# Kernel tuning notes

Hardware: AMD Instinct MI355X
Metric: run time of the kernel (lower is better)

The kernel has to match this reference:

```python
import jax, jax.numpy as jnp
import numpy as np

N = 50000       # nodes
E = 1600000     # edges (avg degree 32)
D = 128         # h_dim
R = 20          # num_rels = 2 * n_labels
L = 2           # RelGraphConv layers (2*n_layers // 2)


def setup_inputs() -> dict:
    key = jax.random.key(0)
    ks = jax.random.split(key, 7)
    node_embeddings = jax.random.normal(ks[0], (N, D), dtype=jnp.float32)
    edge_src = jax.random.randint(ks[1], (E,), 0, N, dtype=jnp.int32)
    edge_dst = jax.random.randint(ks[2], (E,), 0, N, dtype=jnp.int32)
    etypes = jax.random.randint(ks[3], (E,), 0, R, dtype=jnp.int32)
    # per-layer learned params (DGL RelGraphConv, regularizer=None):
    # W: per-relation weight [L, R, D, D]; loop_w: self-loop weight; bias.
    W = jax.random.normal(ks[4], (L, R, D, D), dtype=jnp.float32) / np.float32(np.sqrt(D))
    loop_w = jax.random.normal(ks[5], (L, D, D), dtype=jnp.float32) / np.float32(np.sqrt(D))
    bias = jax.random.normal(ks[6], (L, D), dtype=jnp.float32) * 0.01
    return {
        "node_embeddings": node_embeddings,
        "W": W,
        "loop_w": loop_w,
        "bias": bias,
        "edge_src": edge_src,
        "edge_dst": edge_dst,
        "etypes": etypes,
    }


def reference(node_embeddings, W, loop_w, bias, edge_src, edge_dst, etypes):
    # Stacked RelGraphConv: msg_e = h[src_e] @ W[rel_e]; sum-scatter to dst;
    # h' = agg + h @ loop_w + bias (no activation applied in module forward).
    h = node_embeddings
    num_nodes = h.shape[0]
    for l in range(L):
        # transform every node by every relation once: [N, R, D]
        hW = jnp.einsum('ni,rio->nro', h, W[l])
        msg = hW[edge_src, etypes]                                  # [E, D] gather
        agg = jax.ops.segment_sum(msg, edge_dst, num_segments=num_nodes)
        h = agg + h @ loop_w[l] + bias[l]
    return h
```

## Files before the change

### kernel.cpp

```cpp
#include <hip/hip_runtime.h>
#include <hip/hip_bf16.h>
#include <stdint.h>


#define NN 50000
#define NE 1600000
#define DIM 128
#define NREL 20
#define NRELP 21
#define TILE 16
#define NTILE (NN / TILE)
#define CELLS (NN * NREL)
#define CHB 500
#define CHE (NE / CHB)
#define TT_N (NTILE * CHB)
#define SCAN_EPB 2048
#define NBLK_TT ((TT_N + SCAN_EPB - 1) / SCAN_EPB)
#define SPK_CAP 1024
#define PACKED_ELEMS (2 * NRELP * 4 * 8 * 64 * 8)

typedef __attribute__((ext_vector_type(8))) short short8;
typedef __attribute__((ext_vector_type(8))) _Float16 half8;
typedef __attribute__((ext_vector_type(4))) float f32x4;

__device__ __forceinline__ unsigned short f32_to_f16_raw(float f) {
  union { _Float16 h; unsigned short u; } c;
  c.h = (_Float16)f;
  return c.u;
}

__global__ void cvt_f16_kernel(const float* __restrict__ in,
                               unsigned short* __restrict__ out, int n4) {
  int i = blockIdx.x * 256 + threadIdx.x;
  if (i < n4) {
    float4 f = ((const float4*)in)[i];
    unsigned long long p =
        (unsigned long long)f32_to_f16_raw(f.x)
      | ((unsigned long long)f32_to_f16_raw(f.y) << 16)
      | ((unsigned long long)f32_to_f16_raw(f.z) << 32)
      | ((unsigned long long)f32_to_f16_raw(f.w) << 48);
    __builtin_nontemporal_store(p, (unsigned long long*)out + i);
  }
}

__global__ void pack_w_kernel(const float* __restrict__ W,
                              const float* __restrict__ loop_w,
                              unsigned short* __restrict__ WP) {
  int idx = blockIdx.x * 256 + threadIdx.x;
  if (idx >= PACKED_ELEMS) return;
  int j = idx & 7;       int t = idx >> 3;
  int lane = t & 63;     t >>= 6;
  int nc = t & 7;        t >>= 3;
  int ks = t & 3;        t >>= 2;
  int r = t % NRELP;     int l = t / NRELP;
  int k = ks * 32 + (lane >> 4) * 8 + j;
  int n = nc * 16 + (lane & 15);
  float v = (r < NREL) ? W[(((size_t)l * NREL + r) * DIM + k) * DIM + n]
                       : loop_w[((size_t)l * DIM + k) * DIM + n];
  WP[idx] = f32_to_f16_raw(v);
}

__global__ __launch_bounds__(256) void tile_count_kernel(
    const int* __restrict__ dst, unsigned int* __restrict__ tt) {
  __shared__ unsigned int hist[NTILE];
  for (int i = threadIdx.x; i < NTILE; i += 256) hist[i] = 0u;
  __syncthreads();
  const int base = blockIdx.x * CHE;
  for (int i = base + threadIdx.x; i < base + CHE; i += 256)
    atomicAdd(&hist[dst[i] >> 4], 1u);
  __syncthreads();
  for (int i = threadIdx.x; i < NTILE; i += 256)
    tt[(size_t)i * CHB + blockIdx.x] = hist[i];
}

__global__ void scanA_kernel(const unsigned int* __restrict__ in,
                             unsigned int* __restrict__ out,
                             unsigned int* __restrict__ btot, int n) {
  __shared__ unsigned int buf[256];
  int tid = threadIdx.x;
  int base = blockIdx.x * SCAN_EPB + tid * 8;
  unsigned int v[8], p[8], s = 0;
#pragma unroll
  for (int j = 0; j < 8; ++j) {
    v[j] = (base + j < n) ? in[base + j] : 0u;
    p[j] = s; s += v[j];
  }
  buf[tid] = s;
  __syncthreads();
  for (int d = 1; d < 256; d <<= 1) {
    unsigned int a = (tid >= d) ? buf[tid - d] : 0u;
    __syncthreads();
    buf[tid] += a;
    __syncthreads();
  }
  unsigned int excl = buf[tid] - s;
#pragma unroll
  for (int j = 0; j < 8; ++j)
    if (base + j < n) out[base + j] = excl + p[j];
  if (tid == 255) btot[blockIdx.x] = buf[255];
}

__global__ void scanB_kernel(unsigned int* __restrict__ btot, int nblk) {
  __shared__ unsigned int buf[1024];
  int t = threadIdx.x;
  unsigned int v = (t < nblk) ? btot[t] : 0u;
  buf[t] = v;
  __syncthreads();
  for (int d = 1; d < 1024; d <<= 1) {
    unsigned int a = (t >= d) ? buf[t - d] : 0u;
    __syncthreads();
    buf[t] += a;
    __syncthreads();
  }
  if (t < nblk) btot[t] = buf[t] - v;
}

__global__ void scanC_kernel(const unsigned int* __restrict__ btot,
                             unsigned int* __restrict__ out, int n) {
  int base = blockIdx.x * SCAN_EPB + threadIdx.x * 8;
  unsigned int add = btot[blockIdx.x];
#pragma unroll
  for (int j = 0; j < 8; ++j)
    if (base + j < n) out[base + j] += add;
}

__global__ __launch_bounds__(256) void tile_scatter_kernel(
    const int* __restrict__ src, const int* __restrict__ dst,
    const int* __restrict__ et, const unsigned int* __restrict__ tts,
    unsigned int* __restrict__ ep) {
  __shared__ unsigned int cur[NTILE];
  for (int i = threadIdx.x; i < NTILE; i += 256)
    cur[i] = tts[(size_t)i * CHB + blockIdx.x];
  __syncthreads();
  const int base = blockIdx.x * CHE;
  for (int i = base + threadIdx.x; i < base + CHE; i += 256) {
    int d = dst[i];
    unsigned int pos = atomicAdd(&cur[d >> 4], 1u);
    ep[pos] = (unsigned int)src[i] | ((unsigned int)(d & 15) << 16)
            | ((unsigned int)et[i] << 20);
  }
}

__global__ __launch_bounds__(512) void tile_sort_kernel(
    const unsigned int* __restrict__ ep, const unsigned int* __restrict__ tts,
    unsigned short* __restrict__ es, unsigned int* __restrict__ cofs) {
  __shared__ unsigned int hist[512];
  const int t = threadIdx.x;
  const int tile = blockIdx.x;
  const unsigned int start = tts[(size_t)tile * CHB];
  const unsigned int end = (tile + 1 < NTILE) ? tts[(size_t)(tile + 1) * CHB]
                                              : (unsigned int)NE;
  const int cnt = (int)(end - start);
  hist[t] = 0u;
  __syncthreads();
  for (int i = t; i < cnt; i += 512) {
    unsigned int p = ep[start + i];
    atomicAdd(&hist[((p >> 16) & 15u) * 20u + (p >> 20)], 1u);
  }
  __syncthreads();
  unsigned int own = hist[t];
  for (int d = 1; d < 512; d <<= 1) {
    __syncthreads();
    unsigned int a = (t >= d) ? hist[t - d] : 0u;
    __syncthreads();
    hist[t] += a;
  }
  __syncthreads();
  unsigned int excl = hist[t] - own;
  hist[t] = excl;
  if (t < 320) cofs[(size_t)tile * 320 + t] = start + excl;
  if (tile == NTILE - 1 && t == 0) cofs[CELLS] = (unsigned int)NE;
  __syncthreads();
  for (int i = t; i < cnt; i += 512) {
    unsigned int p = ep[start + i];
    int sub = (int)(((p >> 16) & 15u) * 20u + (p >> 20));
    unsigned int rk = atomicAdd(&hist[sub], 1u);
    es[start + rk] = (unsigned short)(p & 0xffffu);
  }
}

__global__ __launch_bounds__(512, 8) void rgcn_layer_kernel(
    const unsigned short* __restrict__ hb,
    const unsigned short* __restrict__ WP,
    const float* __restrict__ bias,
    int layer,
    const unsigned int* __restrict__ cofs,
    const unsigned short* __restrict__ es,
    float* __restrict__ outf,
    unsigned short* __restrict__ outb)
{
  __shared__ half8 Sb8[TILE * 80];
  __shared__ unsigned int cofs_l[321];
  __shared__ unsigned short spk[SPK_CAP];

  const int tid  = threadIdx.x;
  const int lane = tid & 63;
  const int w    = tid >> 6;
  const int quad = lane >> 4;
  const int m    = lane & 15;
  const int mh8  = m * 8;
  const int half = w >> 2;
  const int g    = (w & 3) * 4 + quad;
  const int dst_base = blockIdx.x * TILE;

  for (int i = tid; i < 321; i += 512) cofs_l[i] = cofs[blockIdx.x * (TILE * NREL) + i];
  __syncthreads();
  const int e0 = (int)cofs_l[0];
  const int etot = (int)cofs_l[320] - e0;
  const bool use_lds = (etot <= SPK_CAP);
  if (use_lds)
    for (int i = tid; i < etot; i += 512) spk[i] = es[e0 + i];
  __syncthreads();

  f32x4 acc = (f32x4){0.f, 0.f, 0.f, 0.f};

  for (int c = 0; c < 5; ++c) {
    if (c < 4) {
      const int cbase = g * NREL + c * 5;
      const int rlA = half ? 2 : 0;
      const int rlB = half ? 5 : 2;
      const int beg    = (int)cofs_l[cbase + rlA] - e0;
      const int endAll = (int)cofs_l[cbase + rlB] - e0;

      half8 a = (half8)(_Float16)0;
      int rl = rlA;
      int nend = (int)cofs_l[cbase + rl + 1] - e0;

      auto flush = [&]() {
        Sb8[g * 80 + ((rl * 16 + m) ^ g)] = a;
        a = (half8)(_Float16)0;
      };
      auto bump = [&](int i) {
        while (i >= nend) {
          flush();
          ++rl;
          nend = (int)cofs_l[cbase + rl + 1] - e0;
        }
      };
      auto run_walk = [&](auto fetch) {
        for (int i = beg; i < endAll; i += 4) {
          const int nrem = endAll - i;
          half8 h0, h1, h2, h3;
          h0 = fetch(i);
          if (nrem > 1) h1 = fetch(i + 1);
          if (nrem > 2) h2 = fetch(i + 2);
          if (nrem > 3) h3 = fetch(i + 3);
          bump(i);      a += h0;
          if (nrem > 1) { bump(i + 1); a += h1; }
          if (nrem > 2) { bump(i + 2); a += h2; }
          if (nrem > 3) { bump(i + 3); a += h3; }
        }
        while (rl < rlB) { flush(); ++rl; }
      };

      if (use_lds) {
        run_walk([&](int i) {
          return *(const half8*)(hb + (size_t)spk[i] * DIM + mh8);
        });
      } else {
        run_walk([&](int i) {
          return *(const half8*)(hb + (size_t)es[e0 + i] * DIM + mh8);
        });
      }
    } else if (half == 0) {
      half8 hv = *(const half8*)(hb + (size_t)(dst_base + g) * DIM + mh8);
      Sb8[g * 80 + (m ^ g)] = hv;
    }
    __syncthreads();

    const int rc = (c == 4) ? 1 : 5;
    for (int rl2 = 0; rl2 < rc; ++rl2) {
      const int r = (c == 4) ? (NRELP - 1) : (c * 5 + rl2);
      const unsigned short* bp =
          WP + ((((size_t)(layer * NRELP + r) * 4) * 8 + w) * 64 + lane) * 8;
#pragma unroll
      for (int ks = 0; ks < 4; ++ks) {
        half8 av = Sb8[m * 80 + ((rl2 * 16 + ks * 4 + quad) ^ m)];
        half8 bv = *(const half8*)(bp + (size_t)ks * 4096);
        acc = __builtin_amdgcn_mfma_f32_16x16x32_f16(av, bv, acc, 0, 0, 0);
      }
    }
    __syncthreads();
  }

  const int col = w * 16 + m;
  const float bv = bias[col];
  if (outb) {
#pragma unroll
    for (int i = 0; i < 4; ++i)
      outb[(size_t)(dst_base + quad * 4 + i) * DIM + col] =
          f32_to_f16_raw(acc[i] + bv);
  } else {
#pragma unroll
    for (int i = 0; i < 4; ++i)
      outf[(size_t)(dst_base + quad * 4 + i) * DIM + col] = acc[i] + bv;
  }
}

extern "C" void kernel_launch(void* const* d_in, const int* in_sizes, int n_in,
                              void* d_out, int out_size, void* d_ws, size_t ws_size,
                              hipStream_t stream) {
  const float* h0     = (const float*)d_in[0];
  const float* W      = (const float*)d_in[1];
  const float* loop_w = (const float*)d_in[2];
  const float* bias   = (const float*)d_in[3];
  const int* esrc     = (const int*)d_in[4];
  const int* edst     = (const int*)d_in[5];
  const int* etyp     = (const int*)d_in[6];
  float* out = (float*)d_out;

  char* ws = (char*)d_ws;
  size_t off = 0;
  auto alloc = [&](size_t bytes) -> void* {
    void* p = ws + off;
    off = (off + bytes + 255) & ~(size_t)255;
    return p;
  };
  unsigned short* hb0   = (unsigned short*)alloc((size_t)NN * DIM * 2);
  unsigned short* hb1   = (unsigned short*)alloc((size_t)NN * DIM * 2);
  unsigned short* WP    = (unsigned short*)alloc((size_t)PACKED_ELEMS * 2);
  unsigned int*   tt    = (unsigned int*)alloc((size_t)(TT_N + 1) * 4);
  unsigned int*   tts   = (unsigned int*)alloc((size_t)(TT_N + 1) * 4);
  unsigned int*   btot  = (unsigned int*)alloc((size_t)NBLK_TT * 4);
  unsigned int*   ep    = (unsigned int*)alloc((size_t)NE * 4);
  unsigned int*   cofs  = (unsigned int*)alloc((size_t)(CELLS + 1) * 4);
  unsigned short* es    = (unsigned short*)alloc((size_t)NE * 2);

  tile_count_kernel<<<CHB, 256, 0, stream>>>(edst, tt);
  scanA_kernel<<<NBLK_TT, 256, 0, stream>>>(tt, tts, btot, TT_N);
  scanB_kernel<<<1, 1024, 0, stream>>>(btot, NBLK_TT);
  scanC_kernel<<<NBLK_TT, 256, 0, stream>>>(btot, tts, TT_N);
  tile_scatter_kernel<<<CHB, 256, 0, stream>>>(esrc, edst, etyp, tts, ep);
  tile_sort_kernel<<<NTILE, 512, 0, stream>>>(ep, tts, es, cofs);

  pack_w_kernel<<<(PACKED_ELEMS + 255) / 256, 256, 0, stream>>>(W, loop_w, WP);
  cvt_f16_kernel<<<(NN * DIM / 4 + 255) / 256, 256, 0, stream>>>(h0, hb0, NN * DIM / 4);

  rgcn_layer_kernel<<<NTILE, 512, 0, stream>>>(hb0, WP, bias, 0, cofs, es,
                                               nullptr, hb1);
  rgcn_layer_kernel<<<NTILE, 512, 0, stream>>>(hb1, WP, bias + DIM, 1, cofs, es,
                                               out, nullptr);
}
```

Measured before the change: 395.7 us.

## Replace three-pass global scan of tile histograms with column scan plus tile scan

Histograms are now stored block-major, and each tile's counts are scanned across blocks by a column-scan kernel. A single-block scan over the per-tile totals then produces the tile start offsets. This replaces the previous three-kernel scan over the full tile×chunk matrix and cuts edge chunks from 500 to 256, reducing launches and scan traffic. The trade-off is less parallelism in the edge count and scatter passes, and a serial per-thread loop over 256 blocks in the column scan.

```diff
diff --git a/kernel.cpp b/kernel.cpp
--- a/kernel.cpp
+++ b/kernel.cpp
@@ -11,11 +11,8 @@
 #define TILE 16
 #define NTILE (NN / TILE)
 #define CELLS (NN * NREL)
-#define CHB 500
+#define CHB 256
 #define CHE (NE / CHB)
-#define TT_N (NTILE * CHB)
-#define SCAN_EPB 2048
-#define NBLK_TT ((TT_N + SCAN_EPB - 1) / SCAN_EPB)
 #define SPK_CAP 1024
 #define PACKED_ELEMS (2 * NRELP * 4 * 8 * 64 * 8)
 
@@ -60,51 +57,46 @@
   WP[idx] = f32_to_f16_raw(v);
 }
 
-__global__ __launch_bounds__(256) void tile_count_kernel(
-    const int* __restrict__ dst, unsigned int* __restrict__ tt) {
-  __shared__ unsigned int hist[NTILE];
-  for (int i = threadIdx.x; i < NTILE; i += 256) hist[i] = 0u;
+__global__ __launch_bounds__(256) void cnt_kernel(
+    const int* __restrict__ dst, unsigned int* __restrict__ cnt) {
+  __shared__ unsigned int h[NTILE];
+  for (int i = threadIdx.x; i < NTILE; i += 256) h[i] = 0u;
   __syncthreads();
   const int base = blockIdx.x * CHE;
   for (int i = base + threadIdx.x; i < base + CHE; i += 256)
-    atomicAdd(&hist[dst[i] >> 4], 1u);
-  __syncthreads();
-  for (int i = threadIdx.x; i < NTILE; i += 256)
-    tt[(size_t)i * CHB + blockIdx.x] = hist[i];
-}
-
-__global__ void scanA_kernel(const unsigned int* __restrict__ in,
-                             unsigned int* __restrict__ out,
-                             unsigned int* __restrict__ btot, int n) {
-  __shared__ unsigned int buf[256];
-  int tid = threadIdx.x;
-  int base = blockIdx.x * SCAN_EPB + tid * 8;
-  unsigned int v[8], p[8], s = 0;
-#pragma unroll
-  for (int j = 0; j < 8; ++j) {
-    v[j] = (base + j < n) ? in[base + j] : 0u;
+    atomicAdd(&h[dst[i] >> 4], 1u);
+  __syncthreads();
+  unsigned int* row = cnt + (size_t)blockIdx.x * NTILE;
+  for (int i = threadIdx.x; i < NTILE; i += 256) row[i] = h[i];
+}
+
+__global__ __launch_bounds__(256) void colscan_kernel(
+    unsigned int* __restrict__ cnt, unsigned int* __restrict__ csum) {
+  int b = blockIdx.x * 256 + threadIdx.x;
+  if (b >= NTILE) return;
+  unsigned int run = 0;
+  for (int blk = 0; blk < CHB; blk += 8) {
+    unsigned int v[8];
+#pragma unroll
+    for (int i = 0; i < 8; ++i) v[i] = cnt[(size_t)(blk + i) * NTILE + b];
+#pragma unroll
+    for (int i = 0; i < 8; ++i) { cnt[(size_t)(blk + i) * NTILE + b] = run; run += v[i]; }
+  }
+  csum[b] = run;
+}
+
+__global__ __launch_bounds__(1024) void scan1_kernel(
+    const unsigned int* __restrict__ csum, unsigned int* __restrict__ starts) {
+  __shared__ unsigned int buf[1024];
+  const int t = threadIdx.x;
+  const int base = t * 4;
+  unsigned int v[4], p[4], s = 0;
+#pragma unroll
+  for (int j = 0; j < 4; ++j) {
+    v[j] = (base + j < NTILE) ? csum[base + j] : 0u;
     p[j] = s; s += v[j];
   }
-  buf[tid] = s;
-  __syncthreads();
-  for (int d = 1; d < 256; d <<= 1) {
-    unsigned int a = (tid >= d) ? buf[tid - d] : 0u;
-    __syncthreads();
-    buf[tid] += a;
-    __syncthreads();
-  }
-  unsigned int excl = buf[tid] - s;
-#pragma unroll
-  for (int j = 0; j < 8; ++j)
-    if (base + j < n) out[base + j] = excl + p[j];
-  if (tid == 255) btot[blockIdx.x] = buf[255];
-}
-
-__global__ void scanB_kernel(unsigned int* __restrict__ btot, int nblk) {
-  __shared__ unsigned int buf[1024];
-  int t = threadIdx.x;
-  unsigned int v = (t < nblk) ? btot[t] : 0u;
-  buf[t] = v;
+  buf[t] = s;
   __syncthreads();
   for (int d = 1; d < 1024; d <<= 1) {
     unsigned int a = (t >= d) ? buf[t - d] : 0u;
@@ -112,25 +104,21 @@
     buf[t] += a;
     __syncthreads();
   }
-  if (t < nblk) btot[t] = buf[t] - v;
-}
-
-__global__ void scanC_kernel(const unsigned int* __restrict__ btot,
-                             unsigned int* __restrict__ out, int n) {
-  int base = blockIdx.x * SCAN_EPB + threadIdx.x * 8;
-  unsigned int add = btot[blockIdx.x];
-#pragma unroll
-  for (int j = 0; j < 8; ++j)
-    if (base + j < n) out[base + j] += add;
-}
-
-__global__ __launch_bounds__(256) void tile_scatter_kernel(
+  unsigned int excl = buf[t] - s;
+#pragma unroll
+  for (int j = 0; j < 4; ++j)
+    if (base + j < NTILE) starts[base + j] = excl + p[j];
+  if (t == 1023) starts[NTILE] = buf[1023];
+}
+
+__global__ __launch_bounds__(256) void scatter_kernel(
     const int* __restrict__ src, const int* __restrict__ dst,
-    const int* __restrict__ et, const unsigned int* __restrict__ tts,
-    unsigned int* __restrict__ ep) {
+    const int* __restrict__ et, const unsigned int* __restrict__ starts,
+    const unsigned int* __restrict__ cnt, unsigned int* __restrict__ ep) {
   __shared__ unsigned int cur[NTILE];
+  const unsigned int* row = cnt + (size_t)blockIdx.x * NTILE;
   for (int i = threadIdx.x; i < NTILE; i += 256)
-    cur[i] = tts[(size_t)i * CHB + blockIdx.x];
+    cur[i] = starts[i] + row[i];
   __syncthreads();
   const int base = blockIdx.x * CHE;
   for (int i = base + threadIdx.x; i < base + CHE; i += 256) {
@@ -142,14 +130,13 @@
 }
 
 __global__ __launch_bounds__(512) void tile_sort_kernel(
-    const unsigned int* __restrict__ ep, const unsigned int* __restrict__ tts,
+    const unsigned int* __restrict__ ep, const unsigned int* __restrict__ starts,
     unsigned short* __restrict__ es, unsigned int* __restrict__ cofs) {
   __shared__ unsigned int hist[512];
   const int t = threadIdx.x;
   const int tile = blockIdx.x;
-  const unsigned int start = tts[(size_t)tile * CHB];
-  const unsigned int end = (tile + 1 < NTILE) ? tts[(size_t)(tile + 1) * CHB]
-                                              : (unsigned int)NE;
+  const unsigned int start = starts[tile];
+  const unsigned int end = starts[tile + 1];
   const int cnt = (int)(end - start);
   hist[t] = 0u;
   __syncthreads();
@@ -319,19 +306,18 @@
   unsigned short* hb0   = (unsigned short*)alloc((size_t)NN * DIM * 2);
   unsigned short* hb1   = (unsigned short*)alloc((size_t)NN * DIM * 2);
   unsigned short* WP    = (unsigned short*)alloc((size_t)PACKED_ELEMS * 2);
-  unsigned int*   tt    = (unsigned int*)alloc((size_t)(TT_N + 1) * 4);
-  unsigned int*   tts   = (unsigned int*)alloc((size_t)(TT_N + 1) * 4);
-  unsigned int*   btot  = (unsigned int*)alloc((size_t)NBLK_TT * 4);
+  unsigned int*   cnt   = (unsigned int*)alloc((size_t)CHB * NTILE * 4);
+  unsigned int*   csum  = (unsigned int*)alloc((size_t)NTILE * 4);
+  unsigned int*   starts= (unsigned int*)alloc((size_t)(NTILE + 1) * 4);
   unsigned int*   ep    = (unsigned int*)alloc((size_t)NE * 4);
   unsigned int*   cofs  = (unsigned int*)alloc((size_t)(CELLS + 1) * 4);
   unsigned short* es    = (unsigned short*)alloc((size_t)NE * 2);
 
-  tile_count_kernel<<<CHB, 256, 0, stream>>>(edst, tt);
-  scanA_kernel<<<NBLK_TT, 256, 0, stream>>>(tt, tts, btot, TT_N);
-  scanB_kernel<<<1, 1024, 0, stream>>>(btot, NBLK_TT);
-  scanC_kernel<<<NBLK_TT, 256, 0, stream>>>(btot, tts, TT_N);
-  tile_scatter_kernel<<<CHB, 256, 0, stream>>>(esrc, edst, etyp, tts, ep);
-  tile_sort_kernel<<<NTILE, 512, 0, stream>>>(ep, tts, es, cofs);
+  cnt_kernel<<<CHB, 256, 0, stream>>>(edst, cnt);
+  colscan_kernel<<<(NTILE + 255) / 256, 256, 0, stream>>>(cnt, csum);
+  scan1_kernel<<<1, 1024, 0, stream>>>(csum, starts);
+  scatter_kernel<<<CHB, 256, 0, stream>>>(esrc, edst, etyp, starts, cnt, ep);
+  tile_sort_kernel<<<NTILE, 512, 0, stream>>>(ep, starts, es, cofs);
 
   pack_w_kernel<<<(PACKED_ELEMS + 255) / 256, 256, 0, stream>>>(W, loop_w, WP);
   cvt_f16_kernel<<<(NN * DIM / 4 + 255) / 256, 256, 0, stream>>>(h0, hb0, NN * DIM / 4);
```

New measurement: 396.3 us. Within noise of the previous version (+0.2%).
